# Optimization experiments

Measured on AMD Instinct MI355X. Metric: run time of the kernel, lower is better.

The kernel has to match this reference:

```python
import jax, jax.numpy as jnp
import numpy as np

N = 50000      # nodes
E = 800000     # edges (avg degree 16)
F_IN = 256     # input feature dim
D = 32         # per-head out dim (layer1)
H1 = 8         # layer1 heads
H2 = 1         # layer2 heads
C = 16         # num_classes


def setup_inputs() -> dict:
    key = jax.random.key(0)
    ks = jax.random.split(key, 11)
    s = 0.05  # weight scale
    return {
        "x": jax.random.normal(ks[0], (N, F_IN), dtype=jnp.float32),
        "src": jax.random.randint(ks[1], (E,), 0, N),
        "dst": jax.random.randint(ks[2], (E,), 0, N),
        "W1": jax.random.normal(ks[3], (F_IN, H1 * D), dtype=jnp.float32) * s,
        "al1": jax.random.normal(ks[4], (H1, D), dtype=jnp.float32) * s,
        "ar1": jax.random.normal(ks[5], (H1, D), dtype=jnp.float32) * s,
        "b1": jnp.zeros((H1 * D,), dtype=jnp.float32),
        "W2": jax.random.normal(ks[6], (H1 * D, H2 * C), dtype=jnp.float32) * s,
        "al2": jax.random.normal(ks[7], (H2, C), dtype=jnp.float32) * s,
        "ar2": jax.random.normal(ks[8], (H2, C), dtype=jnp.float32) * s,
        "b2": jnp.zeros((H2 * C,), dtype=jnp.float32),
    }


def gat_conv(src, dst, x, W, al, ar, b, neg_slope):
    """DGL-style GATConv (eval mode, no dropout, allow_zero_in_degree)."""
    n = x.shape[0]
    H, Dh = al.shape
    h = (x @ W).reshape(n, H, Dh)                      # [N,H,D]
    el = jnp.einsum('nhd,hd->nh', h, al)               # attn_l . h
    er = jnp.einsum('nhd,hd->nh', h, ar)               # attn_r . h
    e = el[src] + er[dst]                              # [E,H]
    e = jnp.where(e > 0, e, neg_slope * e)             # LeakyReLU
    # edge softmax over incoming edges of each dst node, per head
    m = jax.ops.segment_max(e, dst, num_segments=n)    # [N,H]
    m = jnp.where(jnp.isfinite(m), m, 0.0)             # empty segments -> 0
    ex = jnp.exp(e - m[dst])
    denom = jax.ops.segment_sum(ex, dst, num_segments=n)
    alpha = ex / denom[dst]                            # [E,H]
    # weighted scatter-add aggregation
    out = jax.ops.segment_sum(h[src] * alpha[:, :, None], dst, num_segments=n)
    return out + b.reshape(1, H, Dh)                   # [N,H,D]


def reference(x, src, dst, W1, al1, ar1, b1, W2, al2, ar2, b2):
    n = x.shape[0]
    x1 = gat_conv(src, dst, x, W1, al1, ar1, b1, 1.0).reshape(n, -1)  # flatten heads
    x1 = jax.nn.elu(x1)
    x2 = gat_conv(src, dst, x1, W2, al2, ar2, b2, 0.2)[:, 0, :]       # squeeze head dim
    return jax.nn.elu(x2)                                              # [N, C]
```

## Files before the change

### kernel.cpp

```cpp
#include <hip/hip_runtime.h>
#include <math.h>

typedef __attribute__((ext_vector_type(8))) short short8;
typedef __attribute__((ext_vector_type(4))) float f32x4;

__device__ __forceinline__ float elu_f(float v) {
    return v > 0.f ? v : __expf(v) - 1.f;
}

__device__ __forceinline__ unsigned short f2bf(float f) {
    unsigned u = __float_as_uint(f);
    unsigned r = (u + 0x7FFF + ((u >> 16) & 1)) >> 16;
    return (unsigned short)r;
}

__device__ __forceinline__ float bf2f(unsigned short u) {
    return __uint_as_float(((unsigned)u) << 16);
}

__global__ __launch_bounds__(256) void count_prep_kernel(const int* __restrict__ dst, int* __restrict__ cnt,
                                                         int* __restrict__ rank,
                                                         int E, int nCB,
                                                         const float* __restrict__ W1,
                                                         const float* __restrict__ al1, const float* __restrict__ ar1,
                                                         const float* __restrict__ W2,
                                                         const float* __restrict__ al2, const float* __restrict__ ar2,
                                                         unsigned short* __restrict__ W1t,
                                                         unsigned short* __restrict__ W2t) {
    int b = blockIdx.x, t = threadIdx.x;
    if (b < nCB) {
        int e0 = (b * 256 + t) * 4;
        if (e0 + 3 < E) {
            int4 d4 = *(const int4*)&dst[e0];
            int4 r4;
            r4.x = atomicAdd(&cnt[d4.x], 1);
            r4.y = atomicAdd(&cnt[d4.y], 1);
            r4.z = atomicAdd(&cnt[d4.z], 1);
            r4.w = atomicAdd(&cnt[d4.w], 1);
            *(int4*)&rank[e0] = r4;
        } else {
            for (int e = e0; e < E; e++) rank[e] = atomicAdd(&cnt[dst[e]], 1);
        }
        return;
    }
    int bb = b - nCB;
    if (bb < 256) {
        W1t[bb * 256 + t] = f2bf(W1[t * 256 + bb]);
    } else if (bb == 256) {
        int k = t;
        #pragma unroll
        for (int h = 0; h < 8; h++) {
            float sl = 0.f, sr = 0.f;
            #pragma unroll
            for (int d = 0; d < 32; d++) {
                float wv = W1[k * 256 + 32 * h + d];
                sl += wv * al1[h * 32 + d];
                sr += wv * ar1[h * 32 + d];
            }
            W1t[(256 + h) * 256 + k] = f2bf(sl);
            W1t[(264 + h) * 256 + k] = f2bf(sr);
        }
    } else {
        int k = t;
        float sl = 0.f, sr = 0.f;
        #pragma unroll
        for (int c = 0; c < 16; c++) {
            float wv = W2[k * 16 + c];
            W2t[c * 256 + k] = f2bf(wv);
            sl += wv * al2[c];
            sr += wv * ar2[c];
        }
        W2t[16 * 256 + k] = f2bf(sl);
        W2t[17 * 256 + k] = f2bf(sr);
        #pragma unroll
        for (int c = 18; c < 32; c++) W2t[c * 256 + k] = 0;
    }
}

__global__ __launch_bounds__(256) void bsum_kernel(const int* __restrict__ cnt, int* __restrict__ bsum, int n) {
    int b = blockIdx.x, t = threadIdx.x;
    int i0 = b * 1024 + t * 4;
    int s = 0;
    #pragma unroll
    for (int k = 0; k < 4; k++) { int i = i0 + k; if (i < n) s += cnt[i]; }
    #pragma unroll
    for (int m = 1; m < 64; m <<= 1) s += __shfl_xor(s, m);
    __shared__ int ws[4];
    if ((t & 63) == 0) ws[t >> 6] = s;
    __syncthreads();
    if (t == 0) bsum[b] = ws[0] + ws[1] + ws[2] + ws[3];
}

__global__ __launch_bounds__(256) void scan_final_kernel(const int* __restrict__ cnt, const int* __restrict__ bsum,
                                                         int* __restrict__ offs, int n, int nb) {
    int b = blockIdx.x, t = threadIdx.x, lane = t & 63, w = t >> 6;
    __shared__ int ws[4];
    __shared__ int bbase_s;
    int i0 = b * 1024 + t * 4;
    int v[4]; int ts = 0;
    #pragma unroll
    for (int k = 0; k < 4; k++) { int i = i0 + k; v[k] = (i < n) ? cnt[i] : 0; ts += v[k]; }
    int x = ts;
    #pragma unroll
    for (int off = 1; off < 64; off <<= 1) {
        int y = __shfl_up(x, off);
        if (lane >= off) x += y;
    }
    if (lane == 63) ws[w] = x;
    if (w == 0) {
        int bv = (lane < nb) ? bsum[lane] : 0;
        int bx = bv;
        #pragma unroll
        for (int off = 1; off < 64; off <<= 1) {
            int y = __shfl_up(bx, off);
            if (lane >= off) bx += y;
        }
        if (lane == b) bbase_s = bx - bv;
    }
    __syncthreads();
    int wbase = 0;
    #pragma unroll
    for (int k = 0; k < 4; k++) if (k < w) wbase += ws[k];
    int base = bbase_s + wbase + (x - ts);
    #pragma unroll
    for (int k = 0; k < 4; k++) {
        int i = i0 + k;
        if (i < n) offs[i] = base;
        base += v[k];
        if (i == n - 1) offs[n] = base;
    }
}

__global__ __launch_bounds__(256) void scatter_kernel(const int* __restrict__ src, const int* __restrict__ dst,
                                                      const int* __restrict__ rank, const int* __restrict__ offs,
                                                      int* __restrict__ srt, int E) {
    int e0 = (blockIdx.x * 256 + threadIdx.x) * 4;
    if (e0 + 3 < E) {
        int4 s4 = *(const int4*)&src[e0];
        int4 d4 = *(const int4*)&dst[e0];
        int4 r4 = *(const int4*)&rank[e0];
        int px = offs[d4.x];
        int py = offs[d4.y];
        int pz = offs[d4.z];
        int pw = offs[d4.w];
        srt[px + r4.x] = s4.x;
        srt[py + r4.y] = s4.y;
        srt[pz + r4.z] = s4.z;
        srt[pw + r4.w] = s4.w;
    } else {
        for (int e = e0; e < E; e++) {
            srt[offs[dst[e]] + rank[e]] = src[e];
        }
    }
}

#define STR1 40
__global__ __launch_bounds__(512) void gemm1_mfma(const float* __restrict__ x,
                                                  const unsigned short* __restrict__ W1t,
                                                  unsigned short* __restrict__ h,
                                                  float* __restrict__ el1, float* __restrict__ er1, int n) {
    __shared__ unsigned short As[128 * STR1];
    __shared__ unsigned short Bs[272 * STR1];
    int t = threadIdx.x;
    int w = t >> 6, l = t & 63;
    int rb = blockIdx.x * 128;
    f32x4 acc[17] = {};
    int ar = t >> 2;
    int ak = (t & 3) * 8;
    int lr = w * 16 + (l & 15);
    int lg = l >> 4;
    for (int kc = 0; kc < 256; kc += 32) {
        {
            int gr = rb + ar;
            float v[8];
            if (gr < n) {
                f32x4 v0 = *(const f32x4*)&x[(size_t)gr * 256 + kc + ak];
                f32x4 v1 = *(const f32x4*)&x[(size_t)gr * 256 + kc + ak + 4];
                v[0] = v0.x; v[1] = v0.y; v[2] = v0.z; v[3] = v0.w;
                v[4] = v1.x; v[5] = v1.y; v[6] = v1.z; v[7] = v1.w;
            } else {
                #pragma unroll
                for (int i = 0; i < 8; i++) v[i] = 0.f;
            }
            short8 bv;
            #pragma unroll
            for (int i = 0; i < 8; i++) bv[i] = (short)f2bf(v[i]);
            *(short8*)&As[ar * STR1 + ak] = bv;
        }
        #pragma unroll
        for (int i = 0; i < 3; i++) {
            int idx = t + i * 512;
            if (idx < 1088) {
                int bn = idx >> 2;
                int bk = (idx & 3) * 8;
                short8 bv = *(const short8*)&W1t[(size_t)bn * 256 + kc + bk];
                *(short8*)&Bs[bn * STR1 + bk] = bv;
            }
        }
        __syncthreads();
        short8 a = *(short8*)&As[lr * STR1 + lg * 8];
        #pragma unroll
        for (int j = 0; j < 17; j++) {
            short8 b = *(short8*)&Bs[(j * 16 + (l & 15)) * STR1 + lg * 8];
            acc[j] = __builtin_amdgcn_mfma_f32_16x16x32_bf16(a, b, acc[j], 0, 0, 0);
        }
        __syncthreads();
    }
    int r0 = rb + w * 16 + 4 * (l >> 4);
    int c0 = l & 15;
    #pragma unroll
    for (int j = 0; j < 16; j++) {
        #pragma unroll
        for (int i = 0; i < 4; i++) {
            int gr = r0 + i;
            if (gr < n) h[(size_t)gr * 256 + j * 16 + c0] = f2bf(acc[j][i]);
        }
    }
    #pragma unroll
    for (int i = 0; i < 4; i++) {
        int gr = r0 + i;
        if (gr < n) {
            if (c0 < 8) el1[gr * 8 + c0] = acc[16][i];
            else        er1[gr * 8 + (c0 - 8)] = acc[16][i];
        }
    }
}

__global__ __launch_bounds__(256) void agg1_kernel(const unsigned short* __restrict__ h1b,
                                                   const float* __restrict__ el1,
                                                   const float* __restrict__ er1, const float* __restrict__ b1,
                                                   const int* __restrict__ offs, const int* __restrict__ srt,
                                                   unsigned short* __restrict__ x1b, int n0, int n1) {
    int t = threadIdx.x; int lane = t & 63;
    int node = n0 + blockIdx.x * 4 + (t >> 6);
    if (node >= n1) return;
    int beg = offs[node], end = offs[node + 1];
    int q = lane & 31;
    int head = q >> 2;
    int half = lane >> 5;
    float er_h = er1[node * 8 + head];
    float acc[8] = {};
    float dsum = 0.f;
    for (int e = beg + half; e < end; e += 8) {
        int eB = e + 2, eC = e + 4, eD = e + 6;
        bool hB = eB < end, hC = eC < end, hD = eD < end;
        int sA = srt[e];
        int sB = srt[hB ? eB : e];
        int sC = srt[hC ? eC : e];
        int sD = srt[hD ? eD : e];
        float exA = __expf(el1[sA * 8 + head] + er_h);
        float exB = hB ? __expf(el1[sB * 8 + head] + er_h) : 0.f;
        float exC = hC ? __expf(el1[sC * 8 + head] + er_h) : 0.f;
        float exD = hD ? __expf(el1[sD * 8 + head] + er_h) : 0.f;
        short8 hA = *(const short8*)&h1b[(size_t)sA * 256 + q * 8];
        short8 hBv = *(const short8*)&h1b[(size_t)sB * 256 + q * 8];
        short8 hCv = *(const short8*)&h1b[(size_t)sC * 256 + q * 8];
        short8 hDv = *(const short8*)&h1b[(size_t)sD * 256 + q * 8];
        dsum += (exA + exB) + (exC + exD);
        #pragma unroll
        for (int k = 0; k < 8; k++)
            acc[k] += exA * bf2f((unsigned short)hA[k]) + exB * bf2f((unsigned short)hBv[k])
                    + exC * bf2f((unsigned short)hCv[k]) + exD * bf2f((unsigned short)hDv[k]);
    }
    dsum += __shfl_xor(dsum, 32);
    #pragma unroll
    for (int k = 0; k < 8; k++) acc[k] += __shfl_xor(acc[k], 32);
    if (half == 0) {
        float inv = dsum > 0.f ? 1.f / dsum : 0.f;
        f32x4 b0 = *(const f32x4*)&b1[q * 8];
        f32x4 b4 = *(const f32x4*)&b1[q * 8 + 4];
        float o[8];
        o[0] = elu_f(acc[0] * inv + b0.x); o[1] = elu_f(acc[1] * inv + b0.y);
        o[2] = elu_f(acc[2] * inv + b0.z); o[3] = elu_f(acc[3] * inv + b0.w);
        o[4] = elu_f(acc[4] * inv + b4.x); o[5] = elu_f(acc[5] * inv + b4.y);
        o[6] = elu_f(acc[6] * inv + b4.z); o[7] = elu_f(acc[7] * inv + b4.w);
        short8 ov;
        #pragma unroll
        for (int k = 0; k < 8; k++) ov[k] = (short)f2bf(o[k]);
        *(short8*)&x1b[(size_t)node * 256 + q * 8] = ov;
    }
}

__global__ __launch_bounds__(256) void gemm2_mfma(const unsigned short* __restrict__ x1b,
                                                  const unsigned short* __restrict__ W2t,
                                                  float* __restrict__ h2, float* __restrict__ el2,
                                                  float* __restrict__ er2, int n) {
    __shared__ unsigned short As[64 * STR1];
    __shared__ unsigned short Bs[32 * STR1];
    int t = threadIdx.x;
    int w = t >> 6, l = t & 63;
    int rb = blockIdx.x * 64;
    f32x4 acc[2] = {};
    int ar = t >> 2;
    int ak = (t & 3) * 8;
    int lr = w * 16 + (l & 15);
    int lg = l >> 4;
    for (int kc = 0; kc < 256; kc += 32) {
        {
            int gr = rb + ar;
            short8 av = {0, 0, 0, 0, 0, 0, 0, 0};
            if (gr < n) av = *(const short8*)&x1b[(size_t)gr * 256 + kc + ak];
            *(short8*)&As[ar * STR1 + ak] = av;
        }
        if (t < 128) {
            int bn = t >> 2, bk = (t & 3) * 8;
            short8 bv = *(const short8*)&W2t[(size_t)bn * 256 + kc + bk];
            *(short8*)&Bs[bn * STR1 + bk] = bv;
        }
        __syncthreads();
        short8 a = *(short8*)&As[lr * STR1 + lg * 8];
        #pragma unroll
        for (int j = 0; j < 2; j++) {
            short8 b = *(short8*)&Bs[(j * 16 + (l & 15)) * STR1 + lg * 8];
            acc[j] = __builtin_amdgcn_mfma_f32_16x16x32_bf16(a, b, acc[j], 0, 0, 0);
        }
        __syncthreads();
    }
    int r0 = rb + w * 16 + 4 * (l >> 4);
    int c0 = l & 15;
    #pragma unroll
    for (int i = 0; i < 4; i++) {
        int gr = r0 + i;
        if (gr < n) {
            h2[(size_t)gr * 16 + c0] = acc[0][i];
            if (c0 == 0) el2[gr] = acc[1][i];
            else if (c0 == 1) er2[gr] = acc[1][i];
        }
    }
}

__global__ __launch_bounds__(256) void agg2_kernel(const float* __restrict__ h2,
                                                   const float* __restrict__ el2,
                                                   const float* __restrict__ er2, const float* __restrict__ b2,
                                                   const int* __restrict__ offs, const int* __restrict__ srt,
                                                   float* __restrict__ out, int n) {
    int t = threadIdx.x; int lane = t & 63;
    int node = blockIdx.x * 4 + (t >> 6);
    if (node >= n) return;
    int beg = offs[node], end = offs[node + 1];
    int dim = lane & 15, eg = lane >> 4;
    float er_n = er2[node];
    float acc = 0.f, dsum = 0.f;
    for (int e = beg + eg; e < end; e += 16) {
        int eB = e + 4, eC = e + 8, eD = e + 12;
        bool hB = eB < end, hC = eC < end, hD = eD < end;
        int sA = srt[e];
        int sB = srt[hB ? eB : e];
        int sC = srt[hC ? eC : e];
        int sD = srt[hD ? eD : e];
        float evA = el2[sA] + er_n; evA = fmaxf(evA, 0.2f * evA);
        float evB = el2[sB] + er_n; evB = fmaxf(evB, 0.2f * evB);
        float evC = el2[sC] + er_n; evC = fmaxf(evC, 0.2f * evC);
        float evD = el2[sD] + er_n; evD = fmaxf(evD, 0.2f * evD);
        float exA = __expf(evA);
        float exB = hB ? __expf(evB) : 0.f;
        float exC = hC ? __expf(evC) : 0.f;
        float exD = hD ? __expf(evD) : 0.f;
        float hA = h2[(size_t)sA * 16 + dim];
        float hBv = h2[(size_t)sB * 16 + dim];
        float hCv = h2[(size_t)sC * 16 + dim];
        float hDv = h2[(size_t)sD * 16 + dim];
        dsum += (exA + exB) + (exC + exD);
        acc += exA * hA + exB * hBv + exC * hCv + exD * hDv;
    }
    acc += __shfl_xor(acc, 16); acc += __shfl_xor(acc, 32);
    dsum += __shfl_xor(dsum, 16); dsum += __shfl_xor(dsum, 32);
    float inv = dsum > 0.f ? 1.f / dsum : 0.f;
    float o = elu_f(acc * inv + b2[dim]);
    if (lane < 16) out[(size_t)node * 16 + dim] = o;
}

extern "C" void kernel_launch(void* const* d_in, const int* in_sizes, int n_in,
                              void* d_out, int out_size, void* d_ws, size_t ws_size,
                              hipStream_t stream) {
    const float* x   = (const float*)d_in[0];
    const int*   src = (const int*)d_in[1];
    const int*   dst = (const int*)d_in[2];
    const float* W1  = (const float*)d_in[3];
    const float* al1 = (const float*)d_in[4];
    const float* ar1 = (const float*)d_in[5];
    const float* b1  = (const float*)d_in[6];
    const float* W2  = (const float*)d_in[7];
    const float* al2 = (const float*)d_in[8];
    const float* ar2 = (const float*)d_in[9];
    const float* b2  = (const float*)d_in[10];
    const int N = in_sizes[0] / 256;
    const int E = in_sizes[1];

    char* wsp = (char*)d_ws;
    size_t off = 0;
    auto alloc = [&](size_t bytes) -> void* {
        void* p = wsp + off;
        off = (off + bytes + 255) & ~(size_t)255;
        return p;
    };
    unsigned short* h1b = (unsigned short*)alloc((size_t)N * 256 * 2);
    unsigned short* x1b = (unsigned short*)alloc((size_t)N * 256 * 2);
    float* el1 = (float*)alloc((size_t)N * 8 * 4);
    float* er1 = (float*)alloc((size_t)N * 8 * 4);
    float* h2  = (float*)alloc((size_t)N * 16 * 4);
    float* el2 = (float*)alloc((size_t)N * 4);
    float* er2 = (float*)alloc((size_t)N * 4);
    int*   offs = (int*)alloc((size_t)(N + 1) * 4);
    int*   cnt  = (int*)alloc((size_t)N * 4);
    int*   rank = (int*)alloc((size_t)E * 4);
    int*   bsum = (int*)alloc((size_t)64 * 4);
    int*   srt  = (int*)alloc((size_t)E * 4);
    unsigned short* W1t = (unsigned short*)alloc((size_t)272 * 256 * 2);
    unsigned short* W2t = (unsigned short*)alloc((size_t)32 * 256 * 2);

    const int NB  = (N + 1023) / 1024;
    const int nCB = (E + 1023) / 1024;

    (void)hipMemsetAsync(cnt, 0, (size_t)N * 4, stream);
    count_prep_kernel<<<nCB + 258, 256, 0, stream>>>(dst, cnt, rank, E, nCB,
                                                     W1, al1, ar1, W2, al2, ar2, W1t, W2t);
    bsum_kernel<<<NB, 256, 0, stream>>>(cnt, bsum, N);
    scan_final_kernel<<<NB, 256, 0, stream>>>(cnt, bsum, offs, N, NB);
    scatter_kernel<<<(E + 1023) / 1024, 256, 0, stream>>>(src, dst, rank, offs, srt, E);

    gemm1_mfma<<<(N + 127) / 128, 512, 0, stream>>>(x, W1t, h1b, el1, er1, N);
    const int Nh = N / 2;
    agg1_kernel<<<(Nh + 3) / 4, 256, 0, stream>>>(h1b, el1, er1, b1, offs, srt, x1b, 0, Nh);
    agg1_kernel<<<(N - Nh + 3) / 4, 256, 0, stream>>>(h1b, el1, er1, b1, offs, srt, x1b, Nh, N);
    gemm2_mfma<<<(N + 63) / 64, 256, 0, stream>>>(x1b, W2t, h2, el2, er2, N);
    agg2_kernel<<<(N + 3) / 4, 256, 0, stream>>>(h2, el2, er2, b2, offs, srt, (float*)d_out, N);
}
```

Measured before the change: 192.7 us.

## Fuse degree counting into GEMM1 launch and fold memset into prep kernel

Weight prep and zeroing of the count array now run in one kernel, replacing the separate memset. The atomic in-degree counting blocks are interleaved with the first-layer MFMA GEMM blocks in a single launch, so the memory-bound atomics can overlap with the compute-bound GEMM. Count blocks are widened to 512 threads to match the GEMM block size. Count blocks still reserve the GEMM's shared memory, which may limit occupancy for that half of the work.

```diff
diff --git a/kernel.cpp b/kernel.cpp
--- a/kernel.cpp
+++ b/kernel.cpp
@@ -18,18 +18,75 @@
     return __uint_as_float(((unsigned)u) << 16);
 }
 
-__global__ __launch_bounds__(256) void count_prep_kernel(const int* __restrict__ dst, int* __restrict__ cnt,
-                                                         int* __restrict__ rank,
-                                                         int E, int nCB,
-                                                         const float* __restrict__ W1,
-                                                         const float* __restrict__ al1, const float* __restrict__ ar1,
-                                                         const float* __restrict__ W2,
-                                                         const float* __restrict__ al2, const float* __restrict__ ar2,
-                                                         unsigned short* __restrict__ W1t,
-                                                         unsigned short* __restrict__ W2t) {
+__global__ __launch_bounds__(256) void prep_zero_kernel(const float* __restrict__ W1,
+                                                        const float* __restrict__ al1, const float* __restrict__ ar1,
+                                                        const float* __restrict__ W2,
+                                                        const float* __restrict__ al2, const float* __restrict__ ar2,
+                                                        unsigned short* __restrict__ W1t,
+                                                        unsigned short* __restrict__ W2t,
+                                                        int* __restrict__ cnt, int N) {
     int b = blockIdx.x, t = threadIdx.x;
-    if (b < nCB) {
-        int e0 = (b * 256 + t) * 4;
+    if (b < 256) {
+        W1t[b * 256 + t] = f2bf(W1[t * 256 + b]);
+    } else if (b == 256) {
+        int k = t;
+        #pragma unroll
+        for (int h = 0; h < 8; h++) {
+            float sl = 0.f, sr = 0.f;
+            #pragma unroll
+            for (int d = 0; d < 32; d++) {
+                float wv = W1[k * 256 + 32 * h + d];
+                sl += wv * al1[h * 32 + d];
+                sr += wv * ar1[h * 32 + d];
+            }
+            W1t[(256 + h) * 256 + k] = f2bf(sl);
+            W1t[(264 + h) * 256 + k] = f2bf(sr);
+        }
+    } else if (b == 257) {
+        int k = t;
+        float sl = 0.f, sr = 0.f;
+        #pragma unroll
+        for (int c = 0; c < 16; c++) {
+            float wv = W2[k * 16 + c];
+            W2t[c * 256 + k] = f2bf(wv);
+            sl += wv * al2[c];
+            sr += wv * ar2[c];
+        }
+        W2t[16 * 256 + k] = f2bf(sl);
+        W2t[17 * 256 + k] = f2bf(sr);
+        #pragma unroll
+        for (int c = 18; c < 32; c++) W2t[c * 256 + k] = 0;
+    } else {
+        int i0 = (b - 258) * 1024 + t * 4;
+        if (i0 + 3 < N) {
+            *(int4*)&cnt[i0] = make_int4(0, 0, 0, 0);
+        } else {
+            for (int i = i0; i < N; i++) cnt[i] = 0;
+        }
+    }
+}
+
+#define STR1 40
+__global__ __launch_bounds__(512) void gemm1_count_kernel(const int* __restrict__ dst, int* __restrict__ cnt,
+                                                          int* __restrict__ rank, int E, int nCB,
+                                                          const float* __restrict__ x,
+                                                          const unsigned short* __restrict__ W1t,
+                                                          unsigned short* __restrict__ h,
+                                                          float* __restrict__ el1, float* __restrict__ er1,
+                                                          int n, int nGB) {
+    __shared__ unsigned short As[128 * STR1];
+    __shared__ unsigned short Bs[272 * STR1];
+    int b = blockIdx.x, t = threadIdx.x;
+    int nPair = (nCB < nGB) ? nCB : nGB;
+    int type, id;
+    if (b < 2 * nPair) { type = b & 1; id = b >> 1; }
+    else {
+        int r = b - 2 * nPair;
+        if (nCB > nGB) { type = 0; id = nPair + r; }
+        else           { type = 1; id = nPair + r; }
+    }
+    if (type == 0) {
+        int e0 = (id * 512 + t) * 4;
         if (e0 + 3 < E) {
             int4 d4 = *(const int4*)&dst[e0];
             int4 r4;
@@ -43,127 +100,8 @@
         }
         return;
     }
-    int bb = b - nCB;
-    if (bb < 256) {
-        W1t[bb * 256 + t] = f2bf(W1[t * 256 + bb]);
-    } else if (bb == 256) {
-        int k = t;
-        #pragma unroll
-        for (int h = 0; h < 8; h++) {
-            float sl = 0.f, sr = 0.f;
-            #pragma unroll
-            for (int d = 0; d < 32; d++) {
-                float wv = W1[k * 256 + 32 * h + d];
-                sl += wv * al1[h * 32 + d];
-                sr += wv * ar1[h * 32 + d];
-            }
-            W1t[(256 + h) * 256 + k] = f2bf(sl);
-            W1t[(264 + h) * 256 + k] = f2bf(sr);
-        }
-    } else {
-        int k = t;
-        float sl = 0.f, sr = 0.f;
-        #pragma unroll
-        for (int c = 0; c < 16; c++) {
-            float wv = W2[k * 16 + c];
-            W2t[c * 256 + k] = f2bf(wv);
-            sl += wv * al2[c];
-            sr += wv * ar2[c];
-        }
-        W2t[16 * 256 + k] = f2bf(sl);
-        W2t[17 * 256 + k] = f2bf(sr);
-        #pragma unroll
-        for (int c = 18; c < 32; c++) W2t[c * 256 + k] = 0;
-    }
-}
-
-__global__ __launch_bounds__(256) void bsum_kernel(const int* __restrict__ cnt, int* __restrict__ bsum, int n) {
-    int b = blockIdx.x, t = threadIdx.x;
-    int i0 = b * 1024 + t * 4;
-    int s = 0;
-    #pragma unroll
-    for (int k = 0; k < 4; k++) { int i = i0 + k; if (i < n) s += cnt[i]; }
-    #pragma unroll
-    for (int m = 1; m < 64; m <<= 1) s += __shfl_xor(s, m);
-    __shared__ int ws[4];
-    if ((t & 63) == 0) ws[t >> 6] = s;
-    __syncthreads();
-    if (t == 0) bsum[b] = ws[0] + ws[1] + ws[2] + ws[3];
-}
-
-__global__ __launch_bounds__(256) void scan_final_kernel(const int* __restrict__ cnt, const int* __restrict__ bsum,
-                                                         int* __restrict__ offs, int n, int nb) {
-    int b = blockIdx.x, t = threadIdx.x, lane = t & 63, w = t >> 6;
-    __shared__ int ws[4];
-    __shared__ int bbase_s;
-    int i0 = b * 1024 + t * 4;
-    int v[4]; int ts = 0;
-    #pragma unroll
-    for (int k = 0; k < 4; k++) { int i = i0 + k; v[k] = (i < n) ? cnt[i] : 0; ts += v[k]; }
-    int x = ts;
-    #pragma unroll
-    for (int off = 1; off < 64; off <<= 1) {
-        int y = __shfl_up(x, off);
-        if (lane >= off) x += y;
-    }
-    if (lane == 63) ws[w] = x;
-    if (w == 0) {
-        int bv = (lane < nb) ? bsum[lane] : 0;
-        int bx = bv;
-        #pragma unroll
-        for (int off = 1; off < 64; off <<= 1) {
-            int y = __shfl_up(bx, off);
-            if (lane >= off) bx += y;
-        }
-        if (lane == b) bbase_s = bx - bv;
-    }
-    __syncthreads();
-    int wbase = 0;
-    #pragma unroll
-    for (int k = 0; k < 4; k++) if (k < w) wbase += ws[k];
-    int base = bbase_s + wbase + (x - ts);
-    #pragma unroll
-    for (int k = 0; k < 4; k++) {
-        int i = i0 + k;
-        if (i < n) offs[i] = base;
-        base += v[k];
-        if (i == n - 1) offs[n] = base;
-    }
-}
-
-__global__ __launch_bounds__(256) void scatter_kernel(const int* __restrict__ src, const int* __restrict__ dst,
-                                                      const int* __restrict__ rank, const int* __restrict__ offs,
-                                                      int* __restrict__ srt, int E) {
-    int e0 = (blockIdx.x * 256 + threadIdx.x) * 4;
-    if (e0 + 3 < E) {
-        int4 s4 = *(const int4*)&src[e0];
-        int4 d4 = *(const int4*)&dst[e0];
-        int4 r4 = *(const int4*)&rank[e0];
-        int px = offs[d4.x];
-        int py = offs[d4.y];
-        int pz = offs[d4.z];
-        int pw = offs[d4.w];
-        srt[px + r4.x] = s4.x;
-        srt[py + r4.y] = s4.y;
-        srt[pz + r4.z] = s4.z;
-        srt[pw + r4.w] = s4.w;
-    } else {
-        for (int e = e0; e < E; e++) {
-            srt[offs[dst[e]] + rank[e]] = src[e];
-        }
-    }
-}
-
-#define STR1 40
-__global__ __launch_bounds__(512) void gemm1_mfma(const float* __restrict__ x,
-                                                  const unsigned short* __restrict__ W1t,
-                                                  unsigned short* __restrict__ h,
-                                                  float* __restrict__ el1, float* __restrict__ er1, int n) {
-    __shared__ unsigned short As[128 * STR1];
-    __shared__ unsigned short Bs[272 * STR1];
-    int t = threadIdx.x;
     int w = t >> 6, l = t & 63;
-    int rb = blockIdx.x * 128;
+    int rb = id * 128;
     f32x4 acc[17] = {};
     int ar = t >> 2;
     int ak = (t & 3) * 8;
@@ -201,8 +139,8 @@
         short8 a = *(short8*)&As[lr * STR1 + lg * 8];
         #pragma unroll
         for (int j = 0; j < 17; j++) {
-            short8 b = *(short8*)&Bs[(j * 16 + (l & 15)) * STR1 + lg * 8];
-            acc[j] = __builtin_amdgcn_mfma_f32_16x16x32_bf16(a, b, acc[j], 0, 0, 0);
+            short8 bfrag = *(short8*)&Bs[(j * 16 + (l & 15)) * STR1 + lg * 8];
+            acc[j] = __builtin_amdgcn_mfma_f32_16x16x32_bf16(a, bfrag, acc[j], 0, 0, 0);
         }
         __syncthreads();
     }
@@ -222,6 +160,83 @@
         if (gr < n) {
             if (c0 < 8) el1[gr * 8 + c0] = acc[16][i];
             else        er1[gr * 8 + (c0 - 8)] = acc[16][i];
+        }
+    }
+}
+
+__global__ __launch_bounds__(256) void bsum_kernel(const int* __restrict__ cnt, int* __restrict__ bsum, int n) {
+    int b = blockIdx.x, t = threadIdx.x;
+    int i0 = b * 1024 + t * 4;
+    int s = 0;
+    #pragma unroll
+    for (int k = 0; k < 4; k++) { int i = i0 + k; if (i < n) s += cnt[i]; }
+    #pragma unroll
+    for (int m = 1; m < 64; m <<= 1) s += __shfl_xor(s, m);
+    __shared__ int ws[4];
+    if ((t & 63) == 0) ws[t >> 6] = s;
+    __syncthreads();
+    if (t == 0) bsum[b] = ws[0] + ws[1] + ws[2] + ws[3];
+}
+
+__global__ __launch_bounds__(256) void scan_final_kernel(const int* __restrict__ cnt, const int* __restrict__ bsum,
+                                                         int* __restrict__ offs, int n, int nb) {
+    int b = blockIdx.x, t = threadIdx.x, lane = t & 63, w = t >> 6;
+    __shared__ int ws[4];
+    __shared__ int bbase_s;
+    int i0 = b * 1024 + t * 4;
+    int v[4]; int ts = 0;
+    #pragma unroll
+    for (int k = 0; k < 4; k++) { int i = i0 + k; v[k] = (i < n) ? cnt[i] : 0; ts += v[k]; }
+    int x = ts;
+    #pragma unroll
+    for (int off = 1; off < 64; off <<= 1) {
+        int y = __shfl_up(x, off);
+        if (lane >= off) x += y;
+    }
+    if (lane == 63) ws[w] = x;
+    if (w == 0) {
+        int bv = (lane < nb) ? bsum[lane] : 0;
+        int bx = bv;
+        #pragma unroll
+        for (int off = 1; off < 64; off <<= 1) {
+            int y = __shfl_up(bx, off);
+            if (lane >= off) bx += y;
+        }
+        if (lane == b) bbase_s = bx - bv;
+    }
+    __syncthreads();
+    int wbase = 0;
+    #pragma unroll
+    for (int k = 0; k < 4; k++) if (k < w) wbase += ws[k];
+    int base = bbase_s + wbase + (x - ts);
+    #pragma unroll
+    for (int k = 0; k < 4; k++) {
+        int i = i0 + k;
+        if (i < n) offs[i] = base;
+        base += v[k];
+        if (i == n - 1) offs[n] = base;
+    }
+}
+
+__global__ __launch_bounds__(256) void scatter_kernel(const int* __restrict__ src, const int* __restrict__ dst,
+                                                      const int* __restrict__ rank, const int* __restrict__ offs,
+                                                      int* __restrict__ srt, int E) {
+    int e0 = (blockIdx.x * 256 + threadIdx.x) * 4;
+    if (e0 + 3 < E) {
+        int4 s4 = *(const int4*)&src[e0];
+        int4 d4 = *(const int4*)&dst[e0];
+        int4 r4 = *(const int4*)&rank[e0];
+        int px = offs[d4.x];
+        int py = offs[d4.y];
+        int pz = offs[d4.z];
+        int pw = offs[d4.w];
+        srt[px + r4.x] = s4.x;
+        srt[py + r4.y] = s4.y;
+        srt[pz + r4.z] = s4.z;
+        srt[pw + r4.w] = s4.w;
+    } else {
+        for (int e = e0; e < E; e++) {
+            srt[offs[dst[e]] + rank[e]] = src[e];
         }
     }
 }
@@ -311,8 +326,8 @@
         short8 a = *(short8*)&As[lr * STR1 + lg * 8];
         #pragma unroll
         for (int j = 0; j < 2; j++) {
-            short8 b = *(short8*)&Bs[(j * 16 + (l & 15)) * STR1 + lg * 8];
-            acc[j] = __builtin_amdgcn_mfma_f32_16x16x32_bf16(a, b, acc[j], 0, 0, 0);
+            short8 bfrag = *(short8*)&Bs[(j * 16 + (l & 15)) * STR1 + lg * 8];
+            acc[j] = __builtin_amdgcn_mfma_f32_16x16x32_bf16(a, bfrag, acc[j], 0, 0, 0);
         }
         __syncthreads();
     }
@@ -410,16 +425,17 @@
     unsigned short* W2t = (unsigned short*)alloc((size_t)32 * 256 * 2);
 
     const int NB  = (N + 1023) / 1024;
-    const int nCB = (E + 1023) / 1024;
-
-    (void)hipMemsetAsync(cnt, 0, (size_t)N * 4, stream);
-    count_prep_kernel<<<nCB + 258, 256, 0, stream>>>(dst, cnt, rank, E, nCB,
-                                                     W1, al1, ar1, W2, al2, ar2, W1t, W2t);
+    const int NZ  = (N + 1023) / 1024;
+    const int nCB = (E + 2047) / 2048;
+    const int nGB = (N + 127) / 128;
+
+    prep_zero_kernel<<<258 + NZ, 256, 0, stream>>>(W1, al1, ar1, W2, al2, ar2, W1t, W2t, cnt, N);
+    gemm1_count_kernel<<<nCB + nGB, 512, 0, stream>>>(dst, cnt, rank, E, nCB,
+                                                      x, W1t, h1b, el1, er1, N, nGB);
     bsum_kernel<<<NB, 256, 0, stream>>>(cnt, bsum, N);
     scan_final_kernel<<<NB, 256, 0, stream>>>(cnt, bsum, offs, N, NB);
     scatter_kernel<<<(E + 1023) / 1024, 256, 0, stream>>>(src, dst, rank, offs, srt, E);
 
-    gemm1_mfma<<<(N + 127) / 128, 512, 0, stream>>>(x, W1t, h1b, el1, er1, N);
     const int Nh = N / 2;
     agg1_kernel<<<(Nh + 3) / 4, 256, 0, stream>>>(h1b, el1, er1, b1, offs, srt, x1b, 0, Nh);
     agg1_kernel<<<(N - Nh + 3) / 4, 256, 0, stream>>>(h1b, el1, er1, b1, offs, srt, x1b, Nh, N);
```

Result: faster. 182.3 us (-5.4%).
